# Performance work log

Hardware: AMD Instinct MI355X
Metric: run time of the kernel (lower is better)

The kernel has to match this reference:

```python
import jax, jax.numpy as jnp
import numpy as np

B, T, D, H = 4, 2048, 1024, 16
HD = D // H


def setup_inputs() -> dict:
    key = jax.random.key(0)
    k1, k2, k3 = jax.random.split(key, 3)
    x = jax.random.normal(k1, (B, T, D), dtype=jnp.float32)
    # xavier-uniform-like scale for the projections
    s_qkv = float(np.sqrt(6.0 / (D + 3 * D)))
    s_o = float(np.sqrt(6.0 / (D + D)))
    W_qkv = jax.random.uniform(k2, (D, 3 * D), minval=-s_qkv, maxval=s_qkv, dtype=jnp.float32)
    W_o = jax.random.uniform(k3, (D, D), minval=-s_o, maxval=s_o, dtype=jnp.float32)
    b_qkv = jnp.zeros((3 * D,), dtype=jnp.float32)
    b_o = jnp.zeros((D,), dtype=jnp.float32)
    # pad out the last 256 key positions to exercise the padding-mask path
    key_padding_mask = jnp.zeros((B, T), dtype=bool).at[:, -256:].set(True)
    return {"x": x, "W_qkv": W_qkv, "b_qkv": b_qkv, "W_o": W_o, "b_o": b_o,
            "key_padding_mask": key_padding_mask}


def reference(x, W_qkv, b_qkv, W_o, b_o, key_padding_mask):
    Bx, Tx, Dx = x.shape
    # fused QKV projection
    qkv = x @ W_qkv + b_qkv                      # [B,T,3D]
    q, k, v = jnp.split(qkv, 3, axis=-1)
    to_heads = lambda t: t.reshape(Bx, Tx, H, HD).transpose(0, 2, 1, 3)  # [B,H,T,Hd]
    q, k, v = to_heads(q), to_heads(k), to_heads(v)
    scale = 1.0 / np.sqrt(HD).astype(np.float32)
    scores = jnp.einsum('bhqd,bhkd->bhqk', q, k) * scale   # [B,H,T,T]
    causal = jnp.triu(jnp.ones((Tx, Tx), dtype=bool), k=1)  # True above diagonal => masked
    mask = key_padding_mask[:, None, None, :] | causal[None, None, :, :]
    scores = jnp.where(mask, -jnp.inf, scores)
    A = jax.nn.softmax(scores, axis=-1)
    ctx = jnp.einsum('bhqk,bhkd->bhqd', A, v)               # [B,H,T,Hd]
    y = ctx.transpose(0, 2, 1, 3).reshape(Bx, Tx, Dx)
    return y @ W_o + b_o
```

## Files before the change

### kernel.cpp

```cpp
#include <hip/hip_runtime.h>
#include <cstdint>
#include <cstddef>

typedef __bf16 bf16x8 __attribute__((ext_vector_type(8)));
typedef float f32x4 __attribute__((ext_vector_type(4)));
typedef float f32x16 __attribute__((ext_vector_type(16)));
typedef unsigned short u16x4 __attribute__((ext_vector_type(4)));
typedef unsigned int u32x4 __attribute__((ext_vector_type(4)));

__device__ __forceinline__ unsigned short f2bf(float f) {
  union { float f; unsigned u; } v; v.f = f;
  unsigned r = (v.u + 0x7FFF + ((v.u >> 16) & 1)) >> 16;
  return (unsigned short)r;
}

__device__ __forceinline__ unsigned pkbf(float x, float y) {
  unsigned short a = __builtin_bit_cast(unsigned short, (__bf16)x);
  unsigned short b = __builtin_bit_cast(unsigned short, (__bf16)y);
  return (unsigned)a | ((unsigned)b << 16);
}

__device__ __forceinline__ void gl2lds16(const void* g, void* l) {
  __builtin_amdgcn_global_load_lds(
      (const __attribute__((address_space(1))) void*)g,
      (__attribute__((address_space(3))) void*)l,
      16, 0, 0);
}

__global__ __launch_bounds__(256) void prep_fused(
    const float* __restrict__ x, unsigned short* __restrict__ xb,
    const float* __restrict__ Wqkv, unsigned short* __restrict__ WqkvT,
    const float* __restrict__ Wo, unsigned short* __restrict__ WoT,
    const int* __restrict__ mask, int* __restrict__ kparts) {
  __shared__ float t[32][33];
  __shared__ int wred[4];
  const int bid = blockIdx.x, tid = threadIdx.x;
  if (bid < 4096) {
    size_t i = ((size_t)bid * 256 + tid) * 4;
#pragma unroll
    for (int c = 0; c < 2; ++c) {
      float4 v = *(const float4*)(x + i);
      u16x4 o;
      o[0] = f2bf(v.x); o[1] = f2bf(v.y); o[2] = f2bf(v.z); o[3] = f2bf(v.w);
      *(u16x4*)(xb + i) = o;
      i += (size_t)4096 * 256 * 4;
    }
  } else if (bid < 4096 + 3072) {
    const int b2 = bid - 4096;
    const int c0 = (b2 % 96) * 32, r0 = (b2 / 96) * 32;
    const int tx = tid & 31, ty = tid >> 5;
#pragma unroll
    for (int j = 0; j < 4; ++j)
      t[ty + j * 8][tx] = Wqkv[(size_t)(r0 + ty + j * 8) * 3072 + c0 + tx];
    __syncthreads();
#pragma unroll
    for (int j = 0; j < 4; ++j)
      WqkvT[(size_t)(c0 + ty + j * 8) * 1024 + r0 + tx] = f2bf(t[tx][ty + j * 8]);
  } else if (bid < 8192) {
    const int b3 = bid - (4096 + 3072);
    const int c0 = (b3 & 31) * 32, r0 = (b3 >> 5) * 32;
    const int tx = tid & 31, ty = tid >> 5;
#pragma unroll
    for (int j = 0; j < 4; ++j)
      t[ty + j * 8][tx] = Wo[(size_t)(r0 + ty + j * 8) * 1024 + c0 + tx];
    __syncthreads();
#pragma unroll
    for (int j = 0; j < 4; ++j)
      WoT[(size_t)(c0 + ty + j * 8) * 1024 + r0 + tx] = f2bf(t[tx][ty + j * 8]);
  } else {
    const int bi = bid - 8192;
    const int i = bi * 256 + tid;
    int mv = mask[i];
    int key = mv ? 0 : ((i & 2047) + 1);
#pragma unroll
    for (int off = 32; off; off >>= 1) key = max(key, __shfl_xor(key, off, 64));
    if ((tid & 63) == 0) wred[tid >> 6] = key;
    __syncthreads();
    if (tid == 0)
      kparts[bi] = max(max(wred[0], wred[1]), max(wred[2], wred[3]));
  }
}

template <int EPI>
__global__ __launch_bounds__(512, 2) void gemm_bt(
    const unsigned short* __restrict__ A, const unsigned short* __restrict__ Bm,
    const float* __restrict__ bias, float* __restrict__ outF,
    unsigned short* __restrict__ Qb, unsigned short* __restrict__ Kb,
    unsigned short* __restrict__ Vt, int M, int N, int K) {
  extern __shared__ unsigned short lds[];
  const int tid = threadIdx.x;
  const int bm = blockIdx.x * 256;
  const int bn = blockIdx.y * 128;
  const int wave = tid >> 6, lane = tid & 63;
  const int wm4 = wave >> 1, wn2 = wave & 1;
  const int lr = lane & 15, lq = lane >> 4;
  const int NT = K >> 6;

  f32x4 acc[4][4] = {};

  const int tr = tid >> 3, ts = tid & 7;
  const int srcsl = (ts ^ (tr & 7)) << 3;

  auto stage = [&](int buf, int k0) {
#pragma unroll
    for (int r = 0; r < 4; ++r)
      gl2lds16(A + (size_t)(bm + r * 64 + tr) * K + k0 + srcsl,
               lds + buf * 24576 + r * 4096 + tid * 8);
#pragma unroll
    for (int r = 0; r < 2; ++r)
      gl2lds16(Bm + (size_t)(bn + r * 64 + tr) * K + k0 + srcsl,
               lds + buf * 24576 + 16384 + r * 4096 + tid * 8);
  };

  stage(0, 0);
  stage(1, 64);
  int bT = 0, bT2 = 2;
  const int rx = lr & 7;
  for (int T = 0; T < NT; ++T) {
    if (T < NT - 1) {
      asm volatile("s_waitcnt vmcnt(6)" ::: "memory");
    } else {
      asm volatile("s_waitcnt vmcnt(0)" ::: "memory");
    }
    __builtin_amdgcn_s_barrier();
    __builtin_amdgcn_sched_barrier(0);
    if (T + 2 < NT) stage(bT2, (T + 2) << 6);
    const unsigned short* Ab = lds + bT * 24576;
    const unsigned short* Bb = Ab + 16384;
#pragma unroll
    for (int ks = 0; ks < 2; ++ks) {
      bf16x8 afr[4], bfr[4];
#pragma unroll
      for (int mi = 0; mi < 4; ++mi) {
        int row = wm4 * 64 + mi * 16 + lr;
        afr[mi] = *(const bf16x8*)(Ab + row * 64 + ((((ks << 2) | lq) ^ rx) << 3));
      }
#pragma unroll
      for (int nj = 0; nj < 4; ++nj) {
        int row = wn2 * 64 + nj * 16 + lr;
        bfr[nj] = *(const bf16x8*)(Bb + row * 64 + ((((ks << 2) | lq) ^ rx) << 3));
      }
      __builtin_amdgcn_s_setprio(1);
#pragma unroll
      for (int mi = 0; mi < 4; ++mi)
#pragma unroll
        for (int nj = 0; nj < 4; ++nj)
          acc[mi][nj] = __builtin_amdgcn_mfma_f32_16x16x32_bf16(afr[mi], bfr[nj], acc[mi][nj], 0, 0, 0);
      __builtin_amdgcn_s_setprio(0);
    }
    bT = (bT == 2) ? 0 : bT + 1;
    bT2 = (bT2 == 2) ? 0 : bT2 + 1;
  }

#pragma unroll
  for (int mi = 0; mi < 4; ++mi) {
#pragma unroll
    for (int nj = 0; nj < 4; ++nj) {
#pragma unroll
      for (int r = 0; r < 4; ++r) {
        int m = bm + wm4 * 64 + mi * 16 + lq * 4 + r;
        int n = bn + wn2 * 64 + nj * 16 + lr;
        float v = acc[mi][nj][r] + bias[n];
        if (EPI == 0) {
          int b = m >> 11, t = m & 2047;
          int part = n >> 10, d = n & 1023;
          int h = d >> 6, hd = d & 63;
          size_t qk = ((size_t)(b * 16 + h) * 2048 + t) * 64 + hd;
          if (part == 0)      Qb[qk] = f2bf(v * 0.18033688011112042f);
          else if (part == 1) Kb[qk] = f2bf(v);
          else                Vt[((size_t)(b * 16 + h) * 64 + hd) * 2048 + t] = f2bf(v);
        } else {
          outF[(size_t)m * N + n] = v;
        }
      }
    }
  }
}

__global__ __launch_bounds__(256, 4) void flash_attn(
    const unsigned short* __restrict__ Qb, const unsigned short* __restrict__ Kb,
    const unsigned short* __restrict__ Vt, const int* __restrict__ kparts,
    unsigned short* __restrict__ ctx) {
  __shared__ unsigned short lds[24576];

  const int bid = blockIdx.x;
  const int halfg = bid >> 9;
  const int rb = bid & 511;
  const int bh = rb & 63;
  const int j0 = rb >> 6;
  const int j = halfg ? (15 - j0) : j0;
  const int blockQ = j << 7;
  const int b = bh >> 4, h = bh & 15;
  const int tid = threadIdx.x;
  const int wave = tid >> 6, lane = tid & 63;
  const int l31 = lane & 31, hi = lane >> 5;
  const int qw = blockQ + wave * 32;

  const unsigned short* Qh = Qb + (size_t)bh * 2048 * 64;
  const unsigned short* Kh = Kb + (size_t)bh * 2048 * 64;
  const unsigned short* Vh = Vt + (size_t)bh * 64 * 2048;
  unsigned short* ctxBase = ctx + (size_t)b * 2048 * 1024 + h * 64;

  int kmaxRaw = 0;
#pragma unroll
  for (int p = 0; p < 8; ++p) kmaxRaw = max(kmaxRaw, kparts[b * 8 + p]);
  const int kcapC = (kmaxRaw + 63) >> 6;
  const int lastB = min((blockQ + 127) >> 6, kcapC - 1);
  const int diagI = qw >> 6;

  bf16x8 qf[4];
#pragma unroll
  for (int ds = 0; ds < 4; ++ds)
    qf[ds] = *(const bf16x8*)(Qh + (size_t)(qw + l31) * 64 + ds * 16 + hi * 8);

  f32x16 O[2] = {};
  float mR = -1e30f, lR = 0.f;

  const int trow = tid >> 3, tslot = tid & 7;

  auto stage = [&](int bufI, int kcS) {
#pragma unroll
    for (int rnd = 0; rnd < 2; ++rnd) {
      int row = rnd * 32 + trow;
      int sl = tslot ^ (row & 7);
      gl2lds16(Kh + (size_t)(kcS + row) * 64 + sl * 8,
               lds + bufI * 8192 + rnd * 2048 + tid * 8);
      gl2lds16(Vh + (size_t)row * 2048 + kcS + sl * 8,
               lds + bufI * 8192 + 4096 + rnd * 2048 + tid * 8);
    }
  };

  stage(0, 0);
  if (lastB >= 1) stage(1, 64);
  int cb = 0, sb = 2;
  for (int i = 0; i <= lastB; ++i) {
    if (i < lastB) {
      asm volatile("s_waitcnt vmcnt(4)" ::: "memory");
    } else {
      asm volatile("s_waitcnt vmcnt(0)" ::: "memory");
    }
    __builtin_amdgcn_s_barrier();
    __builtin_amdgcn_sched_barrier(0);
    if (i + 2 <= lastB) stage(sb, (i + 2) << 6);
    if (i <= diagI) {
      const int kc = i << 6;
      const unsigned short* Ksb = lds + cb * 8192;
      const unsigned short* Vsb = Ksb + 4096;

      f32x16 S[2] = {};
      __builtin_amdgcn_s_setprio(1);
#pragma unroll
      for (int kt = 0; kt < 2; ++kt) {
        const int row = kt * 32 + l31;
        const int rxk = row & 7;
#pragma unroll
        for (int ds = 0; ds < 4; ++ds) {
          bf16x8 kfr = *(const bf16x8*)(Ksb + row * 64 + (((ds * 2 + hi) ^ rxk) << 3));
          S[kt] = __builtin_amdgcn_mfma_f32_32x32x16_bf16(kfr, qf[ds], S[kt], 0, 0, 0);
        }
      }
      __builtin_amdgcn_s_setprio(0);

      const bool isDiag = (i == diagI);
      if (isDiag || (kc + 64 > kmaxRaw)) {
        const int q = qw + l31;
#pragma unroll
        for (int kt = 0; kt < 2; ++kt)
#pragma unroll
          for (int rr = 0; rr < 16; ++rr) {
            int key = kc + kt * 32 + (rr & 3) + ((rr >> 2) << 3) + (hi << 2);
            if ((isDiag && key > q) || key >= kmaxRaw) S[kt][rr] = -1e30f;
          }
      }

      {
        float v[16];
#pragma unroll
        for (int rr = 0; rr < 16; ++rr) v[rr] = fmaxf(S[0][rr], S[1][rr]);
#pragma unroll
        for (int st = 8; st; st >>= 1)
#pragma unroll
          for (int rr = 0; rr < st; ++rr) v[rr] = fmaxf(v[rr], v[rr + st]);
        float mx = fmaxf(v[0], __shfl_xor(v[0], 32, 64));
        if (__any(mx > mR + 8.0f)) {
          float mnew = fmaxf(mR, mx);
          float a = __builtin_amdgcn_exp2f(mR - mnew);
          mR = mnew;
          lR *= a;
#pragma unroll
          for (int mt = 0; mt < 2; ++mt)
#pragma unroll
            for (int rr = 0; rr < 16; ++rr) O[mt][rr] *= a;
        }
#pragma unroll
        for (int kt = 0; kt < 2; ++kt)
#pragma unroll
          for (int rr = 0; rr < 16; ++rr)
            S[kt][rr] = __builtin_amdgcn_exp2f(S[kt][rr] - mR);
        float sacc[16];
#pragma unroll
        for (int rr = 0; rr < 16; ++rr) sacc[rr] = S[0][rr] + S[1][rr];
#pragma unroll
        for (int st = 8; st; st >>= 1)
#pragma unroll
          for (int rr = 0; rr < st; ++rr) sacc[rr] += sacc[rr + st];
        lR += sacc[0] + __shfl_xor(sacc[0], 32, 64);
      }
      bf16x8 pf[2][2];
#pragma unroll
      for (int kt = 0; kt < 2; ++kt) {
        unsigned a0 = pkbf(S[kt][0], S[kt][1]);
        unsigned a1 = pkbf(S[kt][2], S[kt][3]);
        unsigned b0 = pkbf(S[kt][4], S[kt][5]);
        unsigned b1 = pkbf(S[kt][6], S[kt][7]);
        unsigned c0 = pkbf(S[kt][8], S[kt][9]);
        unsigned c1 = pkbf(S[kt][10], S[kt][11]);
        unsigned d0 = pkbf(S[kt][12], S[kt][13]);
        unsigned d1 = pkbf(S[kt][14], S[kt][15]);
        unsigned s0 = __shfl_xor(hi ? a0 : b0, 32, 64);
        unsigned s1 = __shfl_xor(hi ? a1 : b1, 32, 64);
        unsigned s2 = __shfl_xor(hi ? c0 : d0, 32, 64);
        unsigned s3 = __shfl_xor(hi ? c1 : d1, 32, 64);
        u32x4 f0, f1;
        f0[0] = hi ? s0 : a0; f0[1] = hi ? s1 : a1;
        f0[2] = hi ? b0 : s0; f0[3] = hi ? b1 : s1;
        f1[0] = hi ? s2 : c0; f1[1] = hi ? s3 : c1;
        f1[2] = hi ? d0 : s2; f1[3] = hi ? d1 : s3;
        pf[kt][0] = __builtin_bit_cast(bf16x8, f0);
        pf[kt][1] = __builtin_bit_cast(bf16x8, f1);
      }

      __builtin_amdgcn_s_setprio(1);
      const int vx = l31 & 7;
#pragma unroll
      for (int kt = 0; kt < 2; ++kt)
#pragma unroll
        for (int ks = 0; ks < 2; ++ks) {
          const int slot = kt * 4 + ks * 2 + hi;
          bf16x8 v0 = *(const bf16x8*)(Vsb + l31 * 64 + ((slot ^ vx) << 3));
          bf16x8 v1 = *(const bf16x8*)(Vsb + (32 + l31) * 64 + ((slot ^ vx) << 3));
          O[0] = __builtin_amdgcn_mfma_f32_32x32x16_bf16(v0, pf[kt][ks], O[0], 0, 0, 0);
          O[1] = __builtin_amdgcn_mfma_f32_32x32x16_bf16(v1, pf[kt][ks], O[1], 0, 0, 0);
        }
      __builtin_amdgcn_s_setprio(0);
    }
    cb = (cb == 2) ? 0 : cb + 1;
    sb = (sb == 2) ? 0 : sb + 1;
  }

  {
    float linv = 1.0f / lR;
    const int q = qw + l31;
    unsigned short* cp = ctxBase + (size_t)q * 1024;
#pragma unroll
    for (int mt = 0; mt < 2; ++mt)
#pragma unroll
      for (int g = 0; g < 4; ++g) {
        u16x4 o4;
#pragma unroll
        for (int rr = 0; rr < 4; ++rr) o4[rr] = f2bf(O[mt][4 * g + rr] * linv);
        *(u16x4*)(cp + mt * 32 + 8 * g + 4 * hi) = o4;
      }
  }
}

extern "C" void kernel_launch(void* const* d_in, const int* in_sizes, int n_in,
                              void* d_out, int out_size, void* d_ws, size_t ws_size,
                              hipStream_t stream) {
  const float* x    = (const float*)d_in[0];
  const float* Wqkv = (const float*)d_in[1];
  const float* bqkv = (const float*)d_in[2];
  const float* Wo   = (const float*)d_in[3];
  const float* bo   = (const float*)d_in[4];
  const int*   mask = (const int*)d_in[5];
  float* out = (float*)d_out;

  unsigned short* ws = (unsigned short*)d_ws;
  const size_t SZ_X = (size_t)8192 * 1024;
  unsigned short* xb    = ws;
  unsigned short* WqkvT = xb + SZ_X;
  unsigned short* WoT   = WqkvT + (size_t)3072 * 1024;
  unsigned short* Qb    = WoT + (size_t)1024 * 1024;
  unsigned short* Kb    = Qb + SZ_X;
  unsigned short* Vt    = Kb + SZ_X;
  int*            kparts = (int*)(Vt + SZ_X);
  unsigned short* ctx   = xb;

  static bool inited = false;
  if (!inited) {
    hipFuncSetAttribute((const void*)gemm_bt<0>,
                        hipFuncAttributeMaxDynamicSharedMemorySize, 147456);
    hipFuncSetAttribute((const void*)gemm_bt<1>,
                        hipFuncAttributeMaxDynamicSharedMemorySize, 147456);
    inited = true;
  }

  prep_fused<<<8224, 256, 0, stream>>>(x, xb, Wqkv, WqkvT, Wo, WoT, mask, kparts);
  gemm_bt<0><<<dim3(32, 24), 512, 147456, stream>>>(xb, WqkvT, bqkv, nullptr, Qb, Kb, Vt,
                                                    8192, 3072, 1024);
  flash_attn<<<1024, 256, 0, stream>>>(Qb, Kb, Vt, kparts, ctx);
  gemm_bt<1><<<dim3(32, 8), 512, 147456, stream>>>(ctx, WoT, bo, out, nullptr, nullptr, nullptr,
                                                   8192, 1024, 1024);
}
```

Measured before the change: 268.7 us.

## Add XCD-aware GEMM tile swizzle, double-buffer attention K/V, flatten max reduction

The GEMM grid becomes 1D, and block IDs are remapped so that each XCD processes a compact 4x8 group of output tiles. This is meant to improve L2 reuse of the A and B operands. Flash attention drops from triple to double buffering with a plain __syncthreads, which cuts LDS use per block and could raise occupancy, but it shortens the prefetch distance. The row-max reduction is rewritten as a flatter fmax tree.

```diff
diff --git a/kernel.cpp b/kernel.cpp
--- a/kernel.cpp
+++ b/kernel.cpp
@@ -89,8 +89,11 @@
     unsigned short* __restrict__ Vt, int M, int N, int K) {
   extern __shared__ unsigned short lds[];
   const int tid = threadIdx.x;
-  const int bm = blockIdx.x * 256;
-  const int bn = blockIdx.y * 128;
+  const int lid = blockIdx.x;
+  const int xcd = lid & 7, w = lid >> 3;
+  const int s = w >> 5, a = w & 31;
+  const int bm = (xcd * 4 + (a & 3)) << 8;
+  const int bn = (s * 8 + (a >> 2)) << 7;
   const int wave = tid >> 6, lane = tid & 63;
   const int wm4 = wave >> 1, wn2 = wave & 1;
   const int lr = lane & 15, lq = lane >> 4;
@@ -181,7 +184,7 @@
     const unsigned short* __restrict__ Qb, const unsigned short* __restrict__ Kb,
     const unsigned short* __restrict__ Vt, const int* __restrict__ kparts,
     unsigned short* __restrict__ ctx) {
-  __shared__ unsigned short lds[24576];
+  __shared__ unsigned short lds[16384];
 
   const int bid = blockIdx.x;
   const int halfg = bid >> 9;
@@ -231,20 +234,13 @@
   };
 
   stage(0, 0);
-  if (lastB >= 1) stage(1, 64);
-  int cb = 0, sb = 2;
+  int cur = 0;
   for (int i = 0; i <= lastB; ++i) {
-    if (i < lastB) {
-      asm volatile("s_waitcnt vmcnt(4)" ::: "memory");
-    } else {
-      asm volatile("s_waitcnt vmcnt(0)" ::: "memory");
-    }
-    __builtin_amdgcn_s_barrier();
-    __builtin_amdgcn_sched_barrier(0);
-    if (i + 2 <= lastB) stage(sb, (i + 2) << 6);
+    __syncthreads();
+    if (i < lastB) stage(cur ^ 1, (i + 1) << 6);
     if (i <= diagI) {
       const int kc = i << 6;
-      const unsigned short* Ksb = lds + cb * 8192;
+      const unsigned short* Ksb = lds + cur * 8192;
       const unsigned short* Vsb = Ksb + 4096;
 
       f32x16 S[2] = {};
@@ -274,23 +270,28 @@
       }
 
       {
-        float v[16];
-#pragma unroll
-        for (int rr = 0; rr < 16; ++rr) v[rr] = fmaxf(S[0][rr], S[1][rr]);
-#pragma unroll
-        for (int st = 8; st; st >>= 1)
-#pragma unroll
-          for (int rr = 0; rr < st; ++rr) v[rr] = fmaxf(v[rr], v[rr + st]);
-        float mx = fmaxf(v[0], __shfl_xor(v[0], 32, 64));
+        float a8[8];
+#pragma unroll
+        for (int r = 0; r < 8; ++r)
+          a8[r] = fmaxf(fmaxf(S[0][r], S[0][r + 8]), S[1][r]);
+        float b4[4];
+#pragma unroll
+        for (int r = 0; r < 4; ++r)
+          b4[r] = fmaxf(fmaxf(a8[r], a8[r + 4]), S[1][r + 8]);
+        float c0 = fmaxf(fmaxf(b4[0], b4[2]), S[1][12]);
+        float c1 = fmaxf(fmaxf(b4[1], b4[3]), S[1][13]);
+        float d = fmaxf(fmaxf(c0, c1), S[1][14]);
+        float mxl = fmaxf(d, S[1][15]);
+        float mx = fmaxf(mxl, __shfl_xor(mxl, 32, 64));
         if (__any(mx > mR + 8.0f)) {
           float mnew = fmaxf(mR, mx);
-          float a = __builtin_amdgcn_exp2f(mR - mnew);
+          float aa = __builtin_amdgcn_exp2f(mR - mnew);
           mR = mnew;
-          lR *= a;
+          lR *= aa;
 #pragma unroll
           for (int mt = 0; mt < 2; ++mt)
 #pragma unroll
-            for (int rr = 0; rr < 16; ++rr) O[mt][rr] *= a;
+            for (int rr = 0; rr < 16; ++rr) O[mt][rr] *= aa;
         }
 #pragma unroll
         for (int kt = 0; kt < 2; ++kt)
@@ -344,8 +345,7 @@
         }
       __builtin_amdgcn_s_setprio(0);
     }
-    cb = (cb == 2) ? 0 : cb + 1;
-    sb = (sb == 2) ? 0 : sb + 1;
+    cur ^= 1;
   }
 
   {
@@ -396,9 +396,9 @@
   }
 
   prep_fused<<<8224, 256, 0, stream>>>(x, xb, Wqkv, WqkvT, Wo, WoT, mask, kparts);
-  gemm_bt<0><<<dim3(32, 24), 512, 147456, stream>>>(xb, WqkvT, bqkv, nullptr, Qb, Kb, Vt,
-                                                    8192, 3072, 1024);
+  gemm_bt<0><<<768, 512, 147456, stream>>>(xb, WqkvT, bqkv, nullptr, Qb, Kb, Vt,
+                                           8192, 3072, 1024);
   flash_attn<<<1024, 256, 0, stream>>>(Qb, Kb, Vt, kparts, ctx);
-  gemm_bt<1><<<dim3(32, 8), 512, 147456, stream>>>(ctx, WoT, bo, out, nullptr, nullptr, nullptr,
-                                                   8192, 1024, 1024);
-}
+  gemm_bt<1><<<256, 512, 147456, stream>>>(ctx, WoT, bo, out, nullptr, nullptr, nullptr,
+                                           8192, 1024, 1024);
+}
```

After: 259.9 us. 1.03x faster.
